# Performance work log

Measured on AMD Instinct MI355X. Metric: run time of the kernel, lower is better.

The kernel has to match this reference:

```python
import jax, jax.numpy as jnp
import numpy as np

TEMPERATURE = 0.6
REPETITION_PENALTY = 1.2
VOCAB = 50257


def setup_inputs() -> dict:
    key = jax.random.key(0)
    k1, k2 = jax.random.split(key)
    logits = jax.random.normal(k1, (8, 64, VOCAB), dtype=jnp.float32)
    prev_tokens = jax.random.randint(k2, (64, 200), 0, VOCAB, dtype=jnp.int64)
    return {"logits": logits, "prev_tokens": prev_tokens}


def reference(logits, prev_tokens):
    # logits: [B, S, V]; prev_tokens: [S, P] token ids previously generated per sequence.
    B, S, V = logits.shape
    # set-semantics mask of penalized (seq, token) pairs; duplicate ids collapse to one.
    mask = jnp.zeros((S, V), dtype=bool).at[
        jnp.arange(S)[:, None], prev_tokens
    ].set(True)  # [S, V]
    # torch.all over dim 0: penalty multiplies if all batch logits negative, else divides.
    all_neg = jnp.all(logits < 0, axis=0, keepdims=True)  # [1, S, V]
    penalized = jnp.where(all_neg, logits * REPETITION_PENALTY, logits / REPETITION_PENALTY)
    logits = jnp.where(mask[None, :, :], penalized, logits)
    # Categorical(logits=x) -> probs = softmax(x); temperature scaling fused.
    return jax.nn.softmax(logits / TEMPERATURE, axis=-1)
```

## Files before the change

kernel.cpp:

```cpp
#include <hip/hip_runtime.h>
#include <math.h>

#define BB 8
#define SS 64
#define VV 50257
#define PP 200
#define NW 1571
#define NT 256
#define IT 50
constexpr float RP   = 1.2f;
constexpr float RPI  = 1.0f / 1.2f;
constexpr float TINV = 1.0f / 0.6f;
constexpr float RPT  = RP * TINV;
constexpr float RPIT = RPI * TINV;

typedef float f32x4 __attribute__((ext_vector_type(4)));


__global__ __launch_bounds__(NT) void k_row(
        const float* __restrict__ logits,
        const int*   __restrict__ prev,
        float*       __restrict__ out) {
    __shared__ unsigned lmask[NW];
    __shared__ unsigned lall[NW];
    __shared__ float    red[NT / 64];
    __shared__ float    bcli;

    const int bs  = blockIdx.x;
    const int s   = bs & (SS - 1);
    const int b   = bs >> 6;
    const int tid = threadIdx.x;
    const float* row  = logits + (size_t)bs * VV;
    float*       orow = out    + (size_t)bs * VV;

    const int a0     = (4 - (bs & 3)) & 3;
    const int nb     = (VV - a0) >> 2;
    const int tail   = VV - a0 - (nb << 2);
    const int tstart = a0 + (nb << 2);
    const f32x4* body = (const f32x4*)(row + a0);
    const bool hh = (tid < a0);
    const bool ht = (tid >= 4 && tid < 4 + tail);

    for (int i = tid; i < NW; i += NT) { lmask[i] = 0u; lall[i] = 0u; }
    __syncthreads();

    int   vtok = -1;
    float lv[BB];
    if (tid < PP) {
        vtok = prev[s * PP + tid];
        #pragma unroll
        for (int j = 0; j < BB; ++j)
            lv[j] = logits[((size_t)(j * SS + s)) * VV + vtok];
    }

    float acc = 0.f;
    #pragma unroll
    for (int k = 0; k < IT; ++k) {
        int i = tid + k * NT;
        if (i < nb) {
            f32x4 x = body[i];
            acc += __expf(x.x * TINV) + __expf(x.y * TINV)
                 + __expf(x.z * TINV) + __expf(x.w * TINV);
        }
    }
    if (hh) acc += __expf(row[tid] * TINV);
    if (ht) acc += __expf(row[tstart + tid - 4] * TINV);

    if (tid < PP) {
        unsigned bit = 1u << (vtok & 31);
        unsigned old = atomicOr(&lmask[vtok >> 5], bit);
        if (!(old & bit)) {
            bool alln = true;
            #pragma unroll
            for (int j = 0; j < BB; ++j) alln = alln && (lv[j] < 0.f);
            if (alln) atomicOr(&lall[vtok >> 5], bit);
            const float ft = alln ? RPT : RPIT;
            acc += __expf(lv[b] * ft) - __expf(lv[b] * TINV);
        }
    }

    #pragma unroll
    for (int off = 1; off < 64; off <<= 1) acc += __shfl_xor(acc, off);
    if ((tid & 63) == 0) red[tid >> 6] = acc;
    __syncthreads();
    if (tid == 0) bcli = 1.0f / ((red[0] + red[1]) + (red[2] + red[3]));
    __syncthreads();
    const float li = bcli;

    f32x4* obody = (f32x4*)(orow + a0);
    #pragma unroll
    for (int k = 0; k < IT; ++k) {
        int i = tid + k * NT;
        if (i < nb) {
            f32x4 x = body[i];
            const int vb = a0 + (i << 2);
            const int w0 = vb >> 5, w3 = (vb + 3) >> 5;
            const unsigned m0 = lmask[w0], A0 = lall[w0];
            const unsigned m3 = lmask[w3], A3 = lall[w3];
            f32x4 o;
            #pragma unroll
            for (int j = 0; j < 4; ++j) {
                const int v = vb + j;
                const unsigned mm = ((v >> 5) == w0) ? m0 : m3;
                const unsigned aa = ((v >> 5) == w0) ? A0 : A3;
                const unsigned sh = (unsigned)v & 31u;
                const bool bit = (mm >> sh) & 1u;
                const bool ab  = (aa >> sh) & 1u;
                const float f  = bit ? (ab ? RPT : RPIT) : TINV;
                o[j] = __expf(x[j] * f) * li;
            }
            __builtin_nontemporal_store(o, &obody[i]);
        }
    }
    if (hh || ht) {
        const int v = hh ? tid : (tstart + tid - 4);
        const unsigned mm = lmask[v >> 5], aa = lall[v >> 5];
        const unsigned sh = (unsigned)v & 31u;
        const bool bit = (mm >> sh) & 1u;
        const bool ab  = (aa >> sh) & 1u;
        const float f  = bit ? (ab ? RPT : RPIT) : TINV;
        __builtin_nontemporal_store(__expf(row[v] * f) * li, &orow[v]);
    }
}

extern "C" void kernel_launch(void* const* d_in, const int* in_sizes, int n_in,
                              void* d_out, int out_size, void* d_ws, size_t ws_size,
                              hipStream_t stream) {
    const float* logits = (const float*)d_in[0];
    const int*   prev   = (const int*)d_in[1];
    float* out = (float*)d_out;

    k_row<<<BB * SS, NT, 0, stream>>>(logits, prev, out);
}
```

Baseline: 198.1 us.

## Split each row across three blocks with cooperative grid sync for softmax

Each row is now split into three chunks, processed by 1536 blocks instead of 512, so more CUs share the exp-sum and write passes. Partial sums and the per-sequence penalty bitmask go to workspace; 64 dedicated blocks compute the mask and the penalty correction sums. A cooperative grid sync, or a two-kernel fallback, separates the reduction from the normalise-and-write pass. This adds grid-wide sync overhead and workspace traffic, and relies on the workspace being large enough and on cooperative launch succeeding.

```diff
diff --git a/kernel.cpp b/kernel.cpp
--- a/kernel.cpp
+++ b/kernel.cpp
@@ -1,5 +1,8 @@
 #include <hip/hip_runtime.h>
+#include <hip/hip_cooperative_groups.h>
 #include <math.h>
+
+namespace cg = cooperative_groups;
 
 #define BB 8
 #define SS 64
@@ -7,7 +10,12 @@
 #define PP 200
 #define NW 1571
 #define NT 256
-#define IT 50
+#define NROW 512
+#define NCH 3
+#define Q 4188
+#define ITQ 17
+#define GRID (NROW * NCH)
+
 constexpr float RP   = 1.2f;
 constexpr float RPI  = 1.0f / 1.2f;
 constexpr float TINV = 1.0f / 0.6f;
@@ -17,6 +25,200 @@
 typedef float f32x4 __attribute__((ext_vector_type(4)));
 
 
+__device__ __forceinline__ void phaseA(
+        int blk, int tid,
+        const float* __restrict__ logits, const int* __restrict__ prev,
+        float* __restrict__ wsum, uint2* __restrict__ bits,
+        unsigned* lmask, unsigned* lall, float* dsum, float* red) {
+    const int row = blk & (NROW - 1);
+    const int cc  = blk >> 9;
+    const int s   = row & (SS - 1);
+    const bool ded = (blk < SS);
+
+    int   vtok = -1;
+    float lv[BB];
+    if (ded) {
+        for (int i = tid; i < NW; i += NT) { lmask[i] = 0u; lall[i] = 0u; }
+        if (tid < BB) dsum[tid] = 0.f;
+        if (tid < PP) {
+            vtok = prev[s * PP + tid];
+            #pragma unroll
+            for (int j = 0; j < BB; ++j)
+                lv[j] = logits[((size_t)(j * SS + s)) * VV + vtok];
+        }
+    }
+
+    const float* rowp = logits + (size_t)row * VV;
+    const int a0   = (4 - (row & 3)) & 3;
+    const int nb   = (VV - a0) >> 2;
+    const int iend = ((cc + 1) * Q < nb) ? (cc + 1) * Q : nb;
+    const f32x4* body = (const f32x4*)(rowp + a0);
+
+    float ax = 0.f, ay = 0.f, az = 0.f, aw = 0.f;
+    #pragma unroll
+    for (int k = 0; k < ITQ; ++k) {
+        int i = cc * Q + k * NT + tid;
+        if (i < iend) {
+            f32x4 x = body[i];
+            ax += __expf(x.x * TINV);
+            ay += __expf(x.y * TINV);
+            az += __expf(x.z * TINV);
+            aw += __expf(x.w * TINV);
+        }
+    }
+    float acc = (ax + ay) + (az + aw);
+    if (cc == 0) {
+        const int tail   = VV - a0 - (nb << 2);
+        const int tstart = a0 + (nb << 2);
+        if (tid < a0)                   acc += __expf(rowp[tid] * TINV);
+        if (tid >= 4 && tid < 4 + tail) acc += __expf(rowp[tstart + tid - 4] * TINV);
+    }
+    #pragma unroll
+    for (int off = 1; off < 64; off <<= 1) acc += __shfl_xor(acc, off);
+    if ((tid & 63) == 0) red[tid >> 6] = acc;
+    __syncthreads();
+    if (tid == 0) wsum[row * 8 + cc] = (red[0] + red[1]) + (red[2] + red[3]);
+
+    if (ded) {
+        bool winner = false;
+        bool alln   = false;
+        if (tid < PP) {
+            unsigned bit = 1u << (vtok & 31);
+            unsigned old = atomicOr(&lmask[vtok >> 5], bit);
+            winner = !(old & bit);
+            if (winner) {
+                alln = true;
+                #pragma unroll
+                for (int j = 0; j < BB; ++j) alln = alln && (lv[j] < 0.f);
+                if (alln) atomicOr(&lall[vtok >> 5], bit);
+            }
+        }
+        const float ft = alln ? RPT : RPIT;
+        #pragma unroll
+        for (int j = 0; j < BB; ++j) {
+            float d = winner ? (__expf(lv[j] * ft) - __expf(lv[j] * TINV)) : 0.f;
+            #pragma unroll
+            for (int off = 1; off < 64; off <<= 1) d += __shfl_xor(d, off);
+            if ((tid & 63) == 0) atomicAdd(&dsum[j], d);
+        }
+        __syncthreads();
+        uint2* brow = bits + (size_t)s * NW;
+        for (int i = tid; i < NW; i += NT)
+            brow[i] = make_uint2(lmask[i], lall[i]);
+        if (tid < BB) wsum[((tid << 6) + s) * 8 + 4] = dsum[tid];
+    }
+}
+
+__device__ __forceinline__ void phaseB(
+        int blk, int tid,
+        const float* __restrict__ logits, const float* __restrict__ wsum,
+        const uint2* __restrict__ bits, float* __restrict__ out,
+        unsigned* lmask, unsigned* lall) {
+    const int row = blk & (NROW - 1);
+    const int cc  = blk >> 9;
+    const int s   = row & (SS - 1);
+    const float* rowp = logits + (size_t)row * VV;
+    float*       orow = out    + (size_t)row * VV;
+    const int a0   = (4 - (row & 3)) & 3;
+    const int nb   = (VV - a0) >> 2;
+    const int iend = ((cc + 1) * Q < nb) ? (cc + 1) * Q : nb;
+    const f32x4* body  = (const f32x4*)(rowp + a0);
+    f32x4*       obody = (f32x4*)(orow + a0);
+    const uint2* brow  = bits + (size_t)s * NW;
+
+    const float* wr = wsum + row * 8;
+    const float li = 1.0f / (((wr[0] + wr[1]) + (wr[2] + wr[3])) + wr[4]);
+
+    const int wlo = (a0 + cc * Q * 4) >> 5;
+    const int whi = (a0 + (iend << 2) - 1) >> 5;
+    const int nwd = whi - wlo + 1;
+    for (int i = tid; i < nwd; i += NT) {
+        uint2 c = brow[wlo + i];
+        lmask[i] = c.x;
+        lall[i]  = c.y;
+    }
+    __syncthreads();
+
+    #pragma unroll
+    for (int k = 0; k < ITQ; ++k) {
+        int i = cc * Q + k * NT + tid;
+        if (i < iend) {
+            f32x4 x = body[i];
+            const int vb = a0 + (i << 2);
+            const int w0 = vb >> 5;
+            const int w3 = (vb + 3) >> 5;
+            const unsigned m0 = lmask[w0 - wlo], A0v = lall[w0 - wlo];
+            const unsigned m3 = lmask[w3 - wlo], A3v = lall[w3 - wlo];
+            f32x4 o;
+            #pragma unroll
+            for (int j = 0; j < 4; ++j) {
+                const int v = vb + j;
+                const unsigned mm = ((v >> 5) == w0) ? m0 : m3;
+                const unsigned aa = ((v >> 5) == w0) ? A0v : A3v;
+                const unsigned sh = (unsigned)v & 31u;
+                const float f = ((mm >> sh) & 1u)
+                              ? (((aa >> sh) & 1u) ? RPT : RPIT) : TINV;
+                o[j] = __expf(x[j] * f) * li;
+            }
+            __builtin_nontemporal_store(o, &obody[i]);
+        }
+    }
+    if (cc == 0) {
+        const int tail   = VV - a0 - (nb << 2);
+        const int tstart = a0 + (nb << 2);
+        if (tid < a0) {
+            const int v = tid;
+            const unsigned sh = (unsigned)v & 31u;
+            const float f = ((lmask[0] >> sh) & 1u)
+                          ? (((lall[0] >> sh) & 1u) ? RPT : RPIT) : TINV;
+            __builtin_nontemporal_store(__expf(rowp[v] * f) * li, &orow[v]);
+        }
+        if (tid >= 4 && tid < 4 + tail) {
+            const int v = tstart + tid - 4;
+            uint2 c = brow[v >> 5];
+            const unsigned sh = (unsigned)v & 31u;
+            const float f = ((c.x >> sh) & 1u)
+                          ? (((c.y >> sh) & 1u) ? RPT : RPIT) : TINV;
+            __builtin_nontemporal_store(__expf(rowp[v] * f) * li, &orow[v]);
+        }
+    }
+}
+
+__global__ __launch_bounds__(NT, 6) void k_coop(
+        const float* __restrict__ logits, const int* __restrict__ prev,
+        float* __restrict__ out, float* __restrict__ wsum,
+        uint2* __restrict__ bits) {
+    __shared__ unsigned lmask[NW];
+    __shared__ unsigned lall[NW];
+    __shared__ float    dsum[BB];
+    __shared__ float    red[NT / 64];
+    const int blk = blockIdx.x, tid = threadIdx.x;
+    phaseA(blk, tid, logits, prev, wsum, bits, lmask, lall, dsum, red);
+    __threadfence();
+    cg::this_grid().sync();
+    phaseB(blk, tid, logits, wsum, bits, out, lmask, lall);
+}
+
+__global__ __launch_bounds__(NT, 6) void k_a(
+        const float* __restrict__ logits, const int* __restrict__ prev,
+        float* __restrict__ wsum, uint2* __restrict__ bits) {
+    __shared__ unsigned lmask[NW];
+    __shared__ unsigned lall[NW];
+    __shared__ float    dsum[BB];
+    __shared__ float    red[NT / 64];
+    phaseA(blockIdx.x, threadIdx.x, logits, prev, wsum, bits,
+           lmask, lall, dsum, red);
+}
+
+__global__ __launch_bounds__(NT, 6) void k_b(
+        const float* __restrict__ logits, const float* __restrict__ wsum,
+        const uint2* __restrict__ bits, float* __restrict__ out) {
+    __shared__ unsigned lmask[NW];
+    __shared__ unsigned lall[NW];
+    phaseB(blockIdx.x, threadIdx.x, logits, wsum, bits, out, lmask, lall);
+}
+
+#define IT 50
 __global__ __launch_bounds__(NT) void k_row(
         const float* __restrict__ logits,
         const int*   __restrict__ prev,
@@ -95,18 +297,17 @@
             f32x4 x = body[i];
             const int vb = a0 + (i << 2);
             const int w0 = vb >> 5, w3 = (vb + 3) >> 5;
-            const unsigned m0 = lmask[w0], A0 = lall[w0];
-            const unsigned m3 = lmask[w3], A3 = lall[w3];
+            const unsigned m0 = lmask[w0], A0v = lall[w0];
+            const unsigned m3 = lmask[w3], A3v = lall[w3];
             f32x4 o;
             #pragma unroll
             for (int j = 0; j < 4; ++j) {
                 const int v = vb + j;
                 const unsigned mm = ((v >> 5) == w0) ? m0 : m3;
-                const unsigned aa = ((v >> 5) == w0) ? A0 : A3;
+                const unsigned aa = ((v >> 5) == w0) ? A0v : A3v;
                 const unsigned sh = (unsigned)v & 31u;
-                const bool bit = (mm >> sh) & 1u;
-                const bool ab  = (aa >> sh) & 1u;
-                const float f  = bit ? (ab ? RPT : RPIT) : TINV;
+                const float f = ((mm >> sh) & 1u)
+                              ? (((aa >> sh) & 1u) ? RPT : RPIT) : TINV;
                 o[j] = __expf(x[j] * f) * li;
             }
             __builtin_nontemporal_store(o, &obody[i]);
@@ -116,9 +317,8 @@
         const int v = hh ? tid : (tstart + tid - 4);
         const unsigned mm = lmask[v >> 5], aa = lall[v >> 5];
         const unsigned sh = (unsigned)v & 31u;
-        const bool bit = (mm >> sh) & 1u;
-        const bool ab  = (aa >> sh) & 1u;
-        const float f  = bit ? (ab ? RPT : RPIT) : TINV;
+        const float f = ((mm >> sh) & 1u)
+                      ? (((aa >> sh) & 1u) ? RPT : RPIT) : TINV;
         __builtin_nontemporal_store(__expf(row[v] * f) * li, &orow[v]);
     }
 }
@@ -130,5 +330,20 @@
     const int*   prev   = (const int*)d_in[1];
     float* out = (float*)d_out;
 
-    k_row<<<BB * SS, NT, 0, stream>>>(logits, prev, out);
-}
+    const size_t need = 16384 + (size_t)SS * NW * sizeof(uint2);
+    if (d_ws != nullptr && ws_size >= need) {
+        float* wsum = (float*)d_ws;
+        uint2* bits = (uint2*)((char*)d_ws + 16384);
+        void* args[] = { (void*)&logits, (void*)&prev, (void*)&out,
+                         (void*)&wsum, (void*)&bits };
+        hipError_t e = hipLaunchCooperativeKernel(
+            reinterpret_cast<const void*>(&k_coop),
+            dim3(GRID), dim3(NT), args, 0, stream);
+        if (e != hipSuccess) {
+            k_a<<<GRID, NT, 0, stream>>>(logits, prev, wsum, bits);
+            k_b<<<GRID, NT, 0, stream>>>(logits, wsum, bits, out);
+        }
+    } else {
+        k_row<<<BB * SS, NT, 0, stream>>>(logits, prev, out);
+    }
+}
```

New measurement: 498.2 us. +151.5%, slower.
